# Optimization experiments

Measured on AMD Instinct MI355X. Metric: run time of the kernel, lower is better.

Reference implementation:

```python
import jax, jax.numpy as jnp
import numpy as np

D_MODEL = 1024
N_HEAD = 16
D_K = D_MODEL // N_HEAD
FF = 4096
EPS = 1e-5


def _linear(x, W, b):
    # torch nn.Linear: y = x @ W.T + b ; W stored [out, in]
    return jnp.einsum('bnd,od->bno', x, W) + b


def _mha(xq, xkv, Wq, bq, Wk, bk, Wv, bv):
    B, N, D = xq.shape
    M = xkv.shape[1]
    q = _linear(xq, Wq, bq).reshape(B, N, N_HEAD, D_K).transpose(0, 2, 1, 3)
    k = _linear(xkv, Wk, bk).reshape(B, M, N_HEAD, D_K).transpose(0, 2, 1, 3)
    v = _linear(xkv, Wv, bv).reshape(B, M, N_HEAD, D_K).transpose(0, 2, 1, 3)
    scores = jnp.einsum('bhnd,bhmd->bhnm', q, k) / np.sqrt(D_K).astype(np.float32)
    attn = jax.nn.softmax(scores, axis=-1)
    out = jnp.einsum('bhnm,bhmd->bhnd', attn, v)
    return out.transpose(0, 2, 1, 3).reshape(B, N, D)


def _layernorm(x, g, b):
    mu = jnp.mean(x, axis=-1, keepdims=True)
    var = jnp.mean((x - mu) ** 2, axis=-1, keepdims=True)
    return (x - mu) * jax.lax.rsqrt(var + EPS) * g + b


def setup_inputs() -> dict:
    key = jax.random.key(0)
    ks = jax.random.split(key, 24)
    s = 0.02
    d = {
        'x': jax.random.normal(ks[0], (8, 1024, D_MODEL), jnp.float32),
        'memory': jax.random.normal(ks[1], (8, 1024, D_MODEL), jnp.float32),
        'Wq1': jax.random.normal(ks[2], (D_MODEL, D_MODEL), jnp.float32) * s,
        'bq1': jnp.zeros((D_MODEL,), jnp.float32),
        'Wk1': jax.random.normal(ks[3], (D_MODEL, D_MODEL), jnp.float32) * s,
        'bk1': jnp.zeros((D_MODEL,), jnp.float32),
        'Wv1': jax.random.normal(ks[4], (D_MODEL, D_MODEL), jnp.float32) * s,
        'bv1': jnp.zeros((D_MODEL,), jnp.float32),
        'Wq2': jax.random.normal(ks[5], (D_MODEL, D_MODEL), jnp.float32) * s,
        'bq2': jnp.zeros((D_MODEL,), jnp.float32),
        'Wk2': jax.random.normal(ks[6], (D_MODEL, D_MODEL), jnp.float32) * s,
        'bk2': jnp.zeros((D_MODEL,), jnp.float32),
        'Wv2': jax.random.normal(ks[7], (D_MODEL, D_MODEL), jnp.float32) * s,
        'bv2': jnp.zeros((D_MODEL,), jnp.float32),
        'W1': jax.random.normal(ks[8], (FF, D_MODEL), jnp.float32) * s,
        'b1': jnp.zeros((FF,), jnp.float32),
        'W2': jax.random.normal(ks[9], (D_MODEL, FF), jnp.float32) * s,
        'b2': jnp.zeros((D_MODEL,), jnp.float32),
        'g1': jnp.ones((D_MODEL,), jnp.float32),
        'be1': jnp.zeros((D_MODEL,), jnp.float32),
        'g2': jnp.ones((D_MODEL,), jnp.float32),
        'be2': jnp.zeros((D_MODEL,), jnp.float32),
        'g3': jnp.ones((D_MODEL,), jnp.float32),
        'be3': jnp.zeros((D_MODEL,), jnp.float32),
    }
    return d


def reference(x, memory, Wq1, bq1, Wk1, bk1, Wv1, bv1,
              Wq2, bq2, Wk2, bk2, Wv2, bv2,
              W1, b1, W2, b2, g1, be1, g2, be2, g3, be3):
    # Post-LN decoder layer, eval mode (dropout = identity), no masks
    x = _layernorm(x + _mha(x, x, Wq1, bq1, Wk1, bk1, Wv1, bv1), g1, be1)
    x = _layernorm(x + _mha(x, memory, Wq2, bq2, Wk2, bk2, Wv2, bv2), g2, be2)
    h = jnp.einsum('hf,bnf->bnh', W2, jax.nn.relu(_linear(x, W1, b1))) + b2
    x = _layernorm(x + h, g3, be3)
    return x
```

## Files before the change

### kernel.cpp

```cpp
#include <hip/hip_runtime.h>
#include <hip/hip_bf16.h>

typedef __attribute__((ext_vector_type(8))) short bf16x8;
typedef __attribute__((ext_vector_type(4))) float f32x4;

#define DEVI static __device__ __forceinline__

constexpr int DM  = 1024;
constexpr int NH  = 16;
constexpr int FFD = 4096;
constexpr int BB  = 8;
constexpr int SEQ = 1024;
constexpr int TT  = BB * SEQ;

DEVI float bf2f(unsigned short u) {
    union { unsigned u32; float f; } v; v.u32 = ((unsigned)u) << 16; return v.f;
}
DEVI unsigned short f2bf(float f) {
    union { float f; unsigned u; } v; v.f = f;
    unsigned x = v.u;
    return (unsigned short)((x + 0x7fffu + ((x >> 16) & 1u)) >> 16);
}

DEVI void async_ld16(void* lds, const void* g) {
    __builtin_amdgcn_global_load_lds(
        (const __attribute__((address_space(1))) unsigned int*)g,
        (__attribute__((address_space(3))) unsigned int*)lds, 16, 0, 0);
}

__global__ __launch_bounds__(256)
void k_cvt_all(const float* __restrict__ s0, unsigned short* __restrict__ d0,
               const float* __restrict__ s1, unsigned short* __restrict__ d1,
               const float* __restrict__ s2, unsigned short* __restrict__ d2,
               const float* __restrict__ s3, unsigned short* __restrict__ d3,
               const float* __restrict__ s4, unsigned short* __restrict__ d4,
               const float* __restrict__ s5, unsigned short* __restrict__ d5,
               const float* __restrict__ s6, unsigned short* __restrict__ d6,
               const float* __restrict__ s7, unsigned short* __restrict__ d7,
               const float* __restrict__ s8, unsigned short* __restrict__ d8,
               const float* __restrict__ s9, unsigned short* __restrict__ d9) {
    int b = blockIdx.x;
    const float* s; unsigned short* d;
    if      (b < 8192)  { s = s0; d = d0; }
    else if (b < 16384) { s = s1; d = d1; b -= 8192; }
    else if (b < 17408) { s = s2; d = d2; b -= 16384; }
    else if (b < 18432) { s = s3; d = d3; b -= 17408; }
    else if (b < 19456) { s = s4; d = d4; b -= 18432; }
    else if (b < 20480) { s = s5; d = d5; b -= 19456; }
    else if (b < 21504) { s = s6; d = d6; b -= 20480; }
    else if (b < 22528) { s = s7; d = d7; b -= 21504; }
    else if (b < 26624) { s = s8; d = d8; b -= 22528; }
    else                { s = s9; d = d9; b -= 26624; }
    const int i = (b * 256 + threadIdx.x) * 4;
    float4 v = *reinterpret_cast<const float4*>(s + i);
    ushort4 o;
    o.x = f2bf(v.x); o.y = f2bf(v.y); o.z = f2bf(v.z); o.w = f2bf(v.w);
    *reinterpret_cast<ushort4*>(d + i) = o;
}

template <int ACT, int BIAS_ROW, int SWZ>
__global__ __launch_bounds__(256)
void k_gemm(const unsigned short* __restrict__ A,
            const unsigned short* __restrict__ W,
            const float* __restrict__ bias1, const float* __restrict__ bias2,
            unsigned short* __restrict__ C,
            int M, int N, int K, int Nsplit) {
    __shared__ __align__(16) unsigned short As[128 * 32];
    __shared__ __align__(16) unsigned short Bs[128 * 32];
    const int tid  = threadIdx.x;
    const int lane = tid & 63, wave = tid >> 6;
    const int wm = wave & 1, wn = wave >> 1;
    const int l15 = lane & 15, quad = lane >> 4;

    int bx, by;
    if (SWZ == 1) {
        const int id = blockIdx.y * gridDim.x + blockIdx.x;
        const int xcd = id & 7, i2 = id >> 3;
        bx = i2 % gridDim.x;
        by = (i2 / gridDim.x) * 8 + xcd;
    } else if (SWZ == 2) {
        const int id = blockIdx.y * gridDim.x + blockIdx.x;
        const int xcd = id & 7, i2 = id >> 3;
        by = i2 % gridDim.y;
        bx = (i2 / gridDim.y) * 8 + xcd;
    } else { bx = blockIdx.x; by = blockIdx.y; }
    const int m0 = by * 128;
    const int n0 = bx * 128;

    f32x4 acc[4][4];
#pragma unroll
    for (int i = 0; i < 4; i++)
#pragma unroll
        for (int j = 0; j < 4; j++) acc[i][j] = (f32x4){0.f, 0.f, 0.f, 0.f};

    const int srow = lane >> 2;
    const int scol = (lane & 3) * 8;
    const unsigned short* Ag = A + (size_t)(m0 + wave * 32 + srow) * K + scol;
    const unsigned short* Wg = W + (size_t)(n0 + wave * 32 + srow) * K + scol;
    unsigned short* Al0 = As + (wave * 32) * 32;
    unsigned short* Al1 = As + (wave * 32 + 16) * 32;
    unsigned short* Bl0 = Bs + (wave * 32) * 32;
    unsigned short* Bl1 = Bs + (wave * 32 + 16) * 32;

    for (int kb = 0; kb < K; kb += 32) {
        __syncthreads();
        async_ld16(Al0, Ag + kb);
        async_ld16(Al1, Ag + (size_t)16 * K + kb);
        async_ld16(Bl0, Wg + kb);
        async_ld16(Bl1, Wg + (size_t)16 * K + kb);
        __syncthreads();
        bf16x8 af[4], bfv[4];
#pragma unroll
        for (int mt = 0; mt < 4; mt++)
            af[mt] = *(const bf16x8*)(As + (wm * 64 + mt * 16 + l15) * 32 + quad * 8);
#pragma unroll
        for (int nt = 0; nt < 4; nt++)
            bfv[nt] = *(const bf16x8*)(Bs + (wn * 64 + nt * 16 + l15) * 32 + quad * 8);
#pragma unroll
        for (int mt = 0; mt < 4; mt++)
#pragma unroll
            for (int nt = 0; nt < 4; nt++)
                acc[mt][nt] = __builtin_amdgcn_mfma_f32_16x16x32_bf16(af[mt], bfv[nt], acc[mt][nt], 0, 0, 0);
    }

#pragma unroll
    for (int mt = 0; mt < 4; mt++)
#pragma unroll
        for (int nt = 0; nt < 4; nt++) {
            const int col = n0 + wn * 64 + nt * 16 + l15;
            float bcol = 0.f;
            if (!BIAS_ROW) bcol = col < Nsplit ? bias1[col] : bias2[col - Nsplit];
#pragma unroll
            for (int r = 0; r < 4; r++) {
                const int row = m0 + wm * 64 + mt * 16 + quad * 4 + r;
                float v = acc[mt][nt][r] + (BIAS_ROW ? bias1[row] : bcol);
                if (ACT == 1) v = v > 0.f ? v : 0.f;
                C[(size_t)row * N + col] = f2bf(v);
            }
        }
}

__global__ __launch_bounds__(256)
void k_attn(const unsigned short* __restrict__ Q,
            const unsigned short* __restrict__ K,
            const unsigned short* __restrict__ Vt,
            unsigned short* __restrict__ O,
            int qld, int kld) {
    constexpr int LDP = 72;
    __shared__ __align__(16) unsigned short Ks[64 * 64];
    __shared__ __align__(16) unsigned short Vs[64 * 64];
    __shared__ __align__(16) unsigned short Ps[4][32 * LDP];
    const int tid  = threadIdx.x;
    const int lane = tid & 63, wave = tid >> 6;
    const int l15 = lane & 15, quad = lane >> 4;
    const int bh = blockIdx.y;
    const int b = bh >> 4, h = bh & 15;
    const int q0 = blockIdx.x * 128 + wave * 32;

    bf16x8 aq[2][2];
#pragma unroll
    for (int ntQ = 0; ntQ < 2; ntQ++)
#pragma unroll
        for (int kc = 0; kc < 2; kc++)
            aq[ntQ][kc] = *(const bf16x8*)(Q + (size_t)(b * SEQ + q0 + ntQ * 16 + l15) * qld
                                             + h * 64 + kc * 32 + quad * 8);

    f32x4 o_[4][2];
#pragma unroll
    for (int i = 0; i < 4; i++)
#pragma unroll
        for (int j = 0; j < 2; j++) o_[i][j] = (f32x4){0.f, 0.f, 0.f, 0.f};
    float m_[2] = {-1e30f, -1e30f}, l_[2] = {0.f, 0.f};

    const int srow  = lane >> 3;
    const int ctrue = (lane & 7) ^ srow;
    const int seg0 = wave, seg1 = wave + 4;
    const unsigned short* Kg = K  + (size_t)(b * SEQ) * kld + h * 64 + ctrue * 8;
    const unsigned short* Vg = Vt + (size_t)(h * 64) * TT + b * SEQ + ctrue * 8;

    for (int kt = 0; kt < SEQ; kt += 64) {
        __syncthreads();
        async_ld16(Ks + seg0 * 512, Kg + (size_t)(kt + seg0 * 8 + srow) * kld);
        async_ld16(Ks + seg1 * 512, Kg + (size_t)(kt + seg1 * 8 + srow) * kld);
        async_ld16(Vs + seg0 * 512, Vg + (size_t)(seg0 * 8 + srow) * TT + kt);
        async_ld16(Vs + seg1 * 512, Vg + (size_t)(seg1 * 8 + srow) * TT + kt);
        __syncthreads();

        f32x4 s[4][2];
#pragma unroll
        for (int i = 0; i < 4; i++)
#pragma unroll
            for (int j = 0; j < 2; j++) s[i][j] = (f32x4){0.f, 0.f, 0.f, 0.f};
#pragma unroll
        for (int kc = 0; kc < 2; kc++)
#pragma unroll
            for (int mtK = 0; mtK < 4; mtK++) {
                const int pos = (kc * 4 + quad) ^ (l15 & 7);
                bf16x8 kf = *(const bf16x8*)(Ks + (mtK * 16 + l15) * 64 + pos * 8);
#pragma unroll
                for (int ntQ = 0; ntQ < 2; ntQ++)
                    s[mtK][ntQ] = __builtin_amdgcn_mfma_f32_16x16x32_bf16(kf, aq[ntQ][kc], s[mtK][ntQ], 0, 0, 0);
            }

#pragma unroll
        for (int ntQ = 0; ntQ < 2; ntQ++) {
            float mx = -1e30f;
#pragma unroll
            for (int mtK = 0; mtK < 4; mtK++)
#pragma unroll
                for (int r = 0; r < 4; r++) mx = fmaxf(mx, s[mtK][ntQ][r]);
            mx = fmaxf(mx, __shfl_xor(mx, 16));
            mx = fmaxf(mx, __shfl_xor(mx, 32));
            const float mnew  = fmaxf(m_[ntQ], mx * 0.125f);
            const float alpha = __expf(m_[ntQ] - mnew);
            m_[ntQ] = mnew;
            float sum = 0.f;
#pragma unroll
            for (int mtK = 0; mtK < 4; mtK++) {
                float p0 = __expf(fmaf(s[mtK][ntQ][0], 0.125f, -mnew));
                float p1 = __expf(fmaf(s[mtK][ntQ][1], 0.125f, -mnew));
                float p2 = __expf(fmaf(s[mtK][ntQ][2], 0.125f, -mnew));
                float p3 = __expf(fmaf(s[mtK][ntQ][3], 0.125f, -mnew));
                sum += (p0 + p1) + (p2 + p3);
                ushort4 pk;
                pk.x = f2bf(p0); pk.y = f2bf(p1); pk.z = f2bf(p2); pk.w = f2bf(p3);
                *(ushort4*)(&Ps[wave][(ntQ * 16 + l15) * LDP + mtK * 16 + quad * 4]) = pk;
            }
            sum += __shfl_xor(sum, 16);
            sum += __shfl_xor(sum, 32);
            l_[ntQ] = l_[ntQ] * alpha + sum;
#pragma unroll
            for (int mtD = 0; mtD < 4; mtD++)
#pragma unroll
                for (int r = 0; r < 4; r++) o_[mtD][ntQ][r] *= alpha;
        }
        __asm__ volatile("s_waitcnt lgkmcnt(0)" ::: "memory");

        bf16x8 pf[2][2];
#pragma unroll
        for (int ntQ = 0; ntQ < 2; ntQ++)
#pragma unroll
            for (int kc2 = 0; kc2 < 2; kc2++)
                pf[ntQ][kc2] = *(const bf16x8*)(&Ps[wave][(ntQ * 16 + l15) * LDP + kc2 * 32 + quad * 8]);
#pragma unroll
        for (int kc2 = 0; kc2 < 2; kc2++)
#pragma unroll
            for (int mtD = 0; mtD < 4; mtD++) {
                const int pos = (kc2 * 4 + quad) ^ (l15 & 7);
                bf16x8 vf = *(const bf16x8*)(Vs + (mtD * 16 + l15) * 64 + pos * 8);
#pragma unroll
                for (int ntQ = 0; ntQ < 2; ntQ++)
                    o_[mtD][ntQ] = __builtin_amdgcn_mfma_f32_16x16x32_bf16(vf, pf[ntQ][kc2], o_[mtD][ntQ], 0, 0, 0);
            }
    }

#pragma unroll
    for (int ntQ = 0; ntQ < 2; ntQ++) {
        const float rl = 1.f / l_[ntQ];
        const size_t tok = (size_t)b * SEQ + q0 + ntQ * 16 + l15;
#pragma unroll
        for (int mtD = 0; mtD < 4; mtD++) {
            ushort4 ov;
            ov.x = f2bf(o_[mtD][ntQ][0] * rl);
            ov.y = f2bf(o_[mtD][ntQ][1] * rl);
            ov.z = f2bf(o_[mtD][ntQ][2] * rl);
            ov.w = f2bf(o_[mtD][ntQ][3] * rl);
            *(ushort4*)(O + tok * DM + h * 64 + mtD * 16 + quad * 4) = ov;
        }
    }
}

__global__ __launch_bounds__(256)
void k_add_ln(const unsigned short* __restrict__ Xa,
              const unsigned short* __restrict__ Xb,
              const float* __restrict__ g, const float* __restrict__ be,
              unsigned short* __restrict__ Y, float* __restrict__ Yf) {
    const int row = blockIdx.x;
    const int base = threadIdx.x * 4;
    const size_t off = (size_t)row * DM + base;
    ushort4 xa = *(const ushort4*)(Xa + off);
    ushort4 xb = *(const ushort4*)(Xb + off);
    float v[4];
    v[0] = bf2f(xa.x) + bf2f(xb.x);
    v[1] = bf2f(xa.y) + bf2f(xb.y);
    v[2] = bf2f(xa.z) + bf2f(xb.z);
    v[3] = bf2f(xa.w) + bf2f(xb.w);
    float s1 = v[0] + v[1] + v[2] + v[3];
    float s2 = v[0]*v[0] + v[1]*v[1] + v[2]*v[2] + v[3]*v[3];
#pragma unroll
    for (int o = 32; o; o >>= 1) { s1 += __shfl_xor(s1, o); s2 += __shfl_xor(s2, o); }
    __shared__ float rs1[4], rs2[4];
    if ((threadIdx.x & 63) == 0) { rs1[threadIdx.x >> 6] = s1; rs2[threadIdx.x >> 6] = s2; }
    __syncthreads();
    s1 = rs1[0] + rs1[1] + rs1[2] + rs1[3];
    s2 = rs2[0] + rs2[1] + rs2[2] + rs2[3];
    const float mu = s1 * (1.f / DM);
    const float var = s2 * (1.f / DM) - mu * mu;
    const float rstd = rsqrtf(var + 1e-5f);
    float y[4];
#pragma unroll
    for (int j = 0; j < 4; j++) y[j] = (v[j] - mu) * rstd * g[base + j] + be[base + j];
    if (Y) {
        ushort4 o;
        o.x = f2bf(y[0]); o.y = f2bf(y[1]); o.z = f2bf(y[2]); o.w = f2bf(y[3]);
        *(ushort4*)(Y + off) = o;
    }
    if (Yf) *(float4*)(Yf + off) = (float4){y[0], y[1], y[2], y[3]};
}

extern "C" void kernel_launch(void* const* d_in, const int* in_sizes, int n_in,
                              void* d_out, int out_size, void* d_ws, size_t ws_size,
                              hipStream_t stream) {
    const float* x    = (const float*)d_in[0];
    const float* mem  = (const float*)d_in[1];
    const float* Wq1  = (const float*)d_in[2];  const float* bq1 = (const float*)d_in[3];
    const float* Wk1  = (const float*)d_in[4];  const float* bk1 = (const float*)d_in[5];
    const float* Wv1  = (const float*)d_in[6];  const float* bv1 = (const float*)d_in[7];
    const float* Wq2  = (const float*)d_in[8];  const float* bq2 = (const float*)d_in[9];
    const float* Wk2  = (const float*)d_in[10]; const float* bk2 = (const float*)d_in[11];
    const float* Wv2  = (const float*)d_in[12]; const float* bv2 = (const float*)d_in[13];
    const float* W1   = (const float*)d_in[14]; const float* b1  = (const float*)d_in[15];
    const float* W2   = (const float*)d_in[16]; const float* b2  = (const float*)d_in[17];
    const float* g1   = (const float*)d_in[18]; const float* be1 = (const float*)d_in[19];
    const float* g2   = (const float*)d_in[20]; const float* be2 = (const float*)d_in[21];
    const float* g3   = (const float*)d_in[22]; const float* be3 = (const float*)d_in[23];
    float* out = (float*)d_out;

    const size_t MiB = 1u << 20;
    char* w = (char*)d_ws;
    unsigned short* Wq1b = (unsigned short*)(w + 0 * MiB);
    unsigned short* Wk1b = (unsigned short*)(w + 2 * MiB);
    unsigned short* Wv1b = (unsigned short*)(w + 4 * MiB);
    unsigned short* Wq2b = (unsigned short*)(w + 6 * MiB);
    unsigned short* Wk2b = (unsigned short*)(w + 8 * MiB);
    unsigned short* Wv2b = (unsigned short*)(w + 10 * MiB);
    unsigned short* W1b  = (unsigned short*)(w + 12 * MiB);
    unsigned short* W2b  = (unsigned short*)(w + 20 * MiB);
    unsigned short* xb   = (unsigned short*)(w + 28 * MiB);
    unsigned short* mb   = (unsigned short*)(w + 44 * MiB);
    unsigned short* QKb  = (unsigned short*)(w + 60 * MiB);
    unsigned short* Qb2  = (unsigned short*)(w + 60 * MiB);
    unsigned short* Kb2  = (unsigned short*)(w + 76 * MiB);
    unsigned short* Vtb  = (unsigned short*)(w + 92 * MiB);
    unsigned short* Ab   = (unsigned short*)(w + 108 * MiB);
    unsigned short* x1b  = (unsigned short*)(w + 124 * MiB);
    unsigned short* x2b  = (unsigned short*)(w + 140 * MiB);
    unsigned short* h1b  = (unsigned short*)(w + 60 * MiB);
    unsigned short* h2b  = (unsigned short*)(w + 124 * MiB);

    const dim3 blk(256);
    k_cvt_all<<<30720, blk, 0, stream>>>(x, xb, mem, mb, Wq1, Wq1b, Wk1, Wk1b,
                                         Wv1, Wv1b, Wq2, Wq2b, Wk2, Wk2b,
                                         Wv2, Wv2b, W1, W1b, W2, W2b);

    const dim3 gD(DM / 128, TT / 128);
    const dim3 gQK(2048 / 128, TT / 128);
    const dim3 gVt(TT / 128, DM / 128);
    const dim3 gF(FFD / 128, TT / 128);
    const dim3 gA(SEQ / 128, BB * NH);

    k_gemm<0,0,1><<<gQK, blk, 0, stream>>>(xb,   Wq1b, bq1, bk1, QKb, TT, 2048, DM, 1024);
    k_gemm<0,1,2><<<gVt, blk, 0, stream>>>(Wv1b, xb,   bv1, bv1, Vtb, DM, TT, DM, TT);
    k_attn<<<gA, blk, 0, stream>>>(QKb, QKb + 1024, Vtb, Ab, 2048, 2048);
    k_add_ln<<<TT, blk, 0, stream>>>(xb, Ab, g1, be1, x1b, nullptr);
    k_gemm<0,0,1><<<gD,  blk, 0, stream>>>(x1b,  Wq2b, bq2, bq2, Qb2, TT, DM, DM, DM);
    k_gemm<0,0,1><<<gD,  blk, 0, stream>>>(mb,   Wk2b, bk2, bk2, Kb2, TT, DM, DM, DM);
    k_gemm<0,1,2><<<gVt, blk, 0, stream>>>(Wv2b, mb,   bv2, bv2, Vtb, DM, TT, DM, TT);
    k_attn<<<gA, blk, 0, stream>>>(Qb2, Kb2, Vtb, Ab, 1024, 1024);
    k_add_ln<<<TT, blk, 0, stream>>>(x1b, Ab, g2, be2, x2b, nullptr);
    k_gemm<1,0,0><<<gF, blk, 0, stream>>>(x2b, W1b, b1, b1, h1b, TT, FFD, DM, FFD);
    k_gemm<0,0,1><<<gD, blk, 0, stream>>>(h1b, W2b, b2, b2, h2b, TT, DM, FFD, DM);
    k_add_ln<<<TT, blk, 0, stream>>>(x2b, h2b, g3, be3, nullptr, out);
}
```

Before: 733.2 us.

## Double-buffer GEMM LDS tiles to overlap global loads with MFMA

The GEMM kernel now keeps two LDS buffers per operand and issues the async loads for the next K tile before running the MFMAs on the current tile. This halves the barriers per K step and hides global load latency behind compute. The LDS tile layout is changed so each lane's fragment is contiguous, and the FFN up-projection GEMM switches to the XCD-aware block swizzle. LDS use doubles, which may reduce occupancy, and the loop assumes K is a multiple of 64.

```diff
diff --git a/kernel.cpp b/kernel.cpp
--- a/kernel.cpp
+++ b/kernel.cpp
@@ -58,6 +58,32 @@
     *reinterpret_cast<ushort4*>(d + i) = o;
 }
 
+DEVI void gemm_step(const unsigned short* Ac, const unsigned short* Bc,
+                    unsigned short* An, unsigned short* Bn,
+                    const unsigned short* Ag, const unsigned short* Wg,
+                    size_t K16, int ko, bool pref, int so,
+                    int wm, int wn, int quad, int l15, f32x4 acc[4][4]) {
+    __syncthreads();
+    if (pref) {
+        async_ld16(An + so,       Ag + ko);
+        async_ld16(An + so + 512, Ag + K16 + ko);
+        async_ld16(Bn + so,       Wg + ko);
+        async_ld16(Bn + so + 512, Wg + K16 + ko);
+    }
+    bf16x8 af[4], bfv[4];
+#pragma unroll
+    for (int mt = 0; mt < 4; mt++)
+        af[mt] = *(const bf16x8*)(Ac + (wm * 4 + mt) * 512 + quad * 128 + l15 * 8);
+#pragma unroll
+    for (int nt = 0; nt < 4; nt++)
+        bfv[nt] = *(const bf16x8*)(Bc + (wn * 4 + nt) * 512 + quad * 128 + l15 * 8);
+#pragma unroll
+    for (int mt = 0; mt < 4; mt++)
+#pragma unroll
+        for (int nt = 0; nt < 4; nt++)
+            acc[mt][nt] = __builtin_amdgcn_mfma_f32_16x16x32_bf16(af[mt], bfv[nt], acc[mt][nt], 0, 0, 0);
+}
+
 template <int ACT, int BIAS_ROW, int SWZ>
 __global__ __launch_bounds__(256)
 void k_gemm(const unsigned short* __restrict__ A,
@@ -65,8 +91,8 @@
             const float* __restrict__ bias1, const float* __restrict__ bias2,
             unsigned short* __restrict__ C,
             int M, int N, int K, int Nsplit) {
-    __shared__ __align__(16) unsigned short As[128 * 32];
-    __shared__ __align__(16) unsigned short Bs[128 * 32];
+    __shared__ __align__(16) unsigned short As[2][128 * 32];
+    __shared__ __align__(16) unsigned short Bs[2][128 * 32];
     const int tid  = threadIdx.x;
     const int lane = tid & 63, wave = tid >> 6;
     const int wm = wave & 1, wn = wave >> 1;
@@ -93,34 +119,24 @@
 #pragma unroll
         for (int j = 0; j < 4; j++) acc[i][j] = (f32x4){0.f, 0.f, 0.f, 0.f};
 
-    const int srow = lane >> 2;
-    const int scol = (lane & 3) * 8;
-    const unsigned short* Ag = A + (size_t)(m0 + wave * 32 + srow) * K + scol;
-    const unsigned short* Wg = W + (size_t)(n0 + wave * 32 + srow) * K + scol;
-    unsigned short* Al0 = As + (wave * 32) * 32;
-    unsigned short* Al1 = As + (wave * 32 + 16) * 32;
-    unsigned short* Bl0 = Bs + (wave * 32) * 32;
-    unsigned short* Bl1 = Bs + (wave * 32 + 16) * 32;
-
-    for (int kb = 0; kb < K; kb += 32) {
-        __syncthreads();
-        async_ld16(Al0, Ag + kb);
-        async_ld16(Al1, Ag + (size_t)16 * K + kb);
-        async_ld16(Bl0, Wg + kb);
-        async_ld16(Bl1, Wg + (size_t)16 * K + kb);
-        __syncthreads();
-        bf16x8 af[4], bfv[4];
-#pragma unroll
-        for (int mt = 0; mt < 4; mt++)
-            af[mt] = *(const bf16x8*)(As + (wm * 64 + mt * 16 + l15) * 32 + quad * 8);
-#pragma unroll
-        for (int nt = 0; nt < 4; nt++)
-            bfv[nt] = *(const bf16x8*)(Bs + (wn * 64 + nt * 16 + l15) * 32 + quad * 8);
-#pragma unroll
-        for (int mt = 0; mt < 4; mt++)
-#pragma unroll
-            for (int nt = 0; nt < 4; nt++)
-                acc[mt][nt] = __builtin_amdgcn_mfma_f32_16x16x32_bf16(af[mt], bfv[nt], acc[mt][nt], 0, 0, 0);
+    const int srow = lane & 15;
+    const int scc  = (lane >> 4) * 8;
+    const unsigned short* Ag = A + (size_t)(m0 + wave * 32 + srow) * K + scc;
+    const unsigned short* Wg = W + (size_t)(n0 + wave * 32 + srow) * K + scc;
+    const size_t K16 = (size_t)16 * K;
+    const int so = wave * 1024;
+
+    async_ld16(As[0] + so,       Ag);
+    async_ld16(As[0] + so + 512, Ag + K16);
+    async_ld16(Bs[0] + so,       Wg);
+    async_ld16(Bs[0] + so + 512, Wg + K16);
+
+    const int nk = K >> 5;
+    for (int kb = 0; kb < nk; kb += 2) {
+        gemm_step(As[0], Bs[0], As[1], Bs[1], Ag, Wg, K16, (kb + 1) << 5, true,
+                  so, wm, wn, quad, l15, acc);
+        gemm_step(As[1], Bs[1], As[0], Bs[0], Ag, Wg, K16, (kb + 2) << 5, kb + 2 < nk,
+                  so, wm, wn, quad, l15, acc);
     }
 
 #pragma unroll
@@ -368,7 +384,7 @@
     k_gemm<0,1,2><<<gVt, blk, 0, stream>>>(Wv2b, mb,   bv2, bv2, Vtb, DM, TT, DM, TT);
     k_attn<<<gA, blk, 0, stream>>>(Qb2, Kb2, Vtb, Ab, 1024, 1024);
     k_add_ln<<<TT, blk, 0, stream>>>(x1b, Ab, g2, be2, x2b, nullptr);
-    k_gemm<1,0,0><<<gF, blk, 0, stream>>>(x2b, W1b, b1, b1, h1b, TT, FFD, DM, FFD);
+    k_gemm<1,0,1><<<gF, blk, 0, stream>>>(x2b, W1b, b1, b1, h1b, TT, FFD, DM, FFD);
     k_gemm<0,0,1><<<gD, blk, 0, stream>>>(h1b, W2b, b2, b2, h2b, TT, DM, FFD, DM);
     k_add_ln<<<TT, blk, 0, stream>>>(x2b, h2b, g3, be3, nullptr, out);
 }
```

Result: slower. 861.8 us (+17.5%).
